# Performance work log

Measured on AMD Instinct MI355X. Metric: run time of the kernel, lower is better.

Reference implementation:

```python
import jax, jax.numpy as jnp
import numpy as np

B, C, H, W = 8, 256, 64, 64
CM = C // 4          # mask channels (theta/phi out) = 64
CI = C - CM          # img channels = 192
EPS = 1e-5


def setup_inputs() -> dict:
    key = jax.random.key(0)
    ks = jax.random.split(key, 12)
    return {
        "x": jax.random.normal(ks[0], (B, C, H, W), dtype=jnp.float32),
        "g_w": jax.random.normal(ks[1], (C, C), dtype=jnp.float32) * 0.05,
        "g_b": jax.random.normal(ks[2], (C,), dtype=jnp.float32) * 0.01,
        "theta_w": jax.random.normal(ks[3], (CM, CM), dtype=jnp.float32) * 0.1,
        "theta_b": jax.random.normal(ks[4], (CM,), dtype=jnp.float32) * 0.01,
        "phi_w": jax.random.normal(ks[5], (CM, CI), dtype=jnp.float32) * 0.06,
        "phi_b": jax.random.normal(ks[6], (CM,), dtype=jnp.float32) * 0.01,
        "W_w": jax.random.normal(ks[7], (C, C), dtype=jnp.float32) * 0.05,
        "W_b": jax.random.normal(ks[8], (C,), dtype=jnp.float32) * 0.01,
        "bn_gamma": jax.random.normal(ks[9], (C,), dtype=jnp.float32) * 0.1 + 1.0,
        "bn_beta": jax.random.normal(ks[10], (C,), dtype=jnp.float32) * 0.01,
        "bn_mean": jax.random.normal(ks[11], (C,), dtype=jnp.float32) * 0.1,
        "bn_var": jnp.ones((C,), dtype=jnp.float32),
    }


def _conv1x1(t, w, b):
    # [B,Cin,H,W] x [Cout,Cin] -> [B,Cout,H,W]
    return jnp.einsum('bchw,oc->bohw', t, w) + b[None, :, None, None]


def _maxpool2(t):
    b, c, h, w = t.shape
    return t.reshape(b, c, h // 2, 2, w // 2, 2).max(axis=(3, 5))


def reference(x, g_w, g_b, theta_w, theta_b, phi_w, phi_b, W_w, W_b,
              bn_gamma, bn_beta, bn_mean, bn_var):
    b, c, h, w = x.shape
    ci = c // 4
    mask_ch = x[:, :ci]          # [B, C/4, H, W]
    img_ch = x[:, ci:]           # [B, 3C/4, H, W]

    # g: conv1x1 then 2x2 maxpool -> [B, C, N'] -> [B, N', C]
    g_x = _maxpool2(_conv1x1(x, g_w, g_b)).reshape(b, c, -1).transpose(0, 2, 1)
    # theta: conv1x1 on mask -> [B, N, C/4]
    theta_x = _conv1x1(mask_ch, theta_w, theta_b).reshape(b, ci, -1).transpose(0, 2, 1)
    # phi: conv1x1 on img then pool -> [B, C/4, N']
    phi_x = _maxpool2(_conv1x1(img_ch, phi_w, phi_b)).reshape(b, ci, -1)

    f = jnp.einsum('bnc,bcm->bnm', theta_x, phi_x)     # [B, N, N']
    f_div_C = jax.nn.softmax(f, axis=-1)
    y = jnp.einsum('bnm,bmc->bnc', f_div_C, g_x)       # [B, N, C]
    y = y.transpose(0, 2, 1).reshape(b, c, h, w)

    W_y = _conv1x1(y, W_w, W_b)
    # BatchNorm (inference form with running stats)
    inv = jax.lax.rsqrt(bn_var + EPS)
    W_y = (W_y - bn_mean[None, :, None, None]) * (inv * bn_gamma)[None, :, None, None] \
          + bn_beta[None, :, None, None]
    return W_y + x
```

## Files before the change

### kernel.cpp

```cpp
#include <hip/hip_runtime.h>
#include <hip/hip_bf16.h>

typedef __hip_bfloat16 bf16;
typedef unsigned short ushort;
typedef unsigned int uint;
typedef __attribute__((ext_vector_type(8))) short short8;
typedef __attribute__((ext_vector_type(4))) float f32x4;

#define Bn 8
#define Cn 256
#define Nn 4096
#define Mn 1024
#define EPSf 1e-5f

__device__ __forceinline__ float b2f(const bf16 v){ return __bfloat162float(v); }
__device__ __forceinline__ ushort f2bu(float f){
  uint u = __float_as_uint(f);
  return (ushort)((u + 0x7FFFu + ((u >> 16) & 1u)) >> 16);
}


__global__ __launch_bounds__(256) void transpose_kernel(
    const float* __restrict__ x, bf16* __restrict__ xT)
{
  __shared__ float xs[64][65];
  const int t = threadIdx.x;
  const int p0 = blockIdx.x*64, c0 = blockIdx.y*64, b = blockIdx.z;
  #pragma unroll
  for (int i = 0; i < 16; ++i) {
    int idx = t + i*256; int cl = idx >> 6, pl = idx & 63;
    xs[cl][pl] = x[((long)(b*Cn) + c0 + cl)*Nn + p0 + pl];
  }
  __syncthreads();
  ushort* xTu = (ushort*)xT;
  #pragma unroll
  for (int i = 0; i < 8; ++i) {
    int idx = t + i*256; int pl = idx >> 5, cp = idx & 31;
    uint u = (uint)f2bu(xs[cp*2][pl]) | ((uint)f2bu(xs[cp*2+1][pl]) << 16);
    *(uint*)(xTu + ((long)(b*Nn) + p0 + pl)*Cn + c0 + cp*2) = u;
  }
}

__global__ __launch_bounds__(256) void wcomb_kernel(
    const float* __restrict__ tw, const float* __restrict__ tb,
    const float* __restrict__ pw, const float* __restrict__ pb,
    const float* __restrict__ gw, const float* __restrict__ gb,
    bf16* __restrict__ Wcomb, float* __restrict__ bcomb)
{
  const int r = blockIdx.x, c = threadIdx.x;
  float v;
  if (r < 64)        v = (c < 64)  ? tw[r*64 + c]            : 0.f;
  else if (r < 128)  v = (c >= 64) ? pw[(r-64)*192 + (c-64)] : 0.f;
  else               v = gw[(r-128)*256 + c];
  Wcomb[r*256 + c] = __float2bfloat16(v);
  if (c == 0)
    bcomb[r] = (r < 64) ? tb[r] : (r < 128) ? pb[r-64] : gb[r-128];
}

__global__ __launch_bounds__(256) void gemm384_kernel(
    const bf16* __restrict__ xT, const bf16* __restrict__ Wcomb,
    const float* __restrict__ bcomb, bf16* __restrict__ Q,
    bf16* __restrict__ K, bf16* __restrict__ Vt)
{
  __shared__ union {
    struct { ushort As[128*40]; ushort Bs[128*40]; } g;
    float Pb[2][128][33];
  } sm;
  const int t = threadIdx.x;
  const int px = blockIdx.x, o0 = blockIdx.y*128, b = blockIdx.z;
  const int p0 = px*128;
  const int lane = t & 63, w = t >> 6;
  const int ql = lane & 15, quad = lane >> 4;
  const int wm = (w & 1)*64, wn = (w >> 1)*64;
  const ushort* xTu = (const ushort*)xT;
  const ushort* Wu  = (const ushort*)Wcomb;

  const int r0 = t >> 2, cq0 = t & 3;
  const int r1 = (t + 256) >> 2, cq1 = (t + 256) & 3;
  const ushort* aSrc0 = xTu + ((long)(b*Nn) + p0 + r0)*Cn + cq0*8;
  const ushort* aSrc1 = xTu + ((long)(b*Nn) + p0 + r1)*Cn + cq1*8;
  const ushort* bSrc0 = Wu + (o0 + r0)*Cn + cq0*8;
  const ushort* bSrc1 = Wu + (o0 + r1)*Cn + cq1*8;

  f32x4 acc[4][4];
  #pragma unroll
  for (int i = 0; i < 4; ++i)
    #pragma unroll
    for (int j = 0; j < 4; ++j) acc[i][j] = (f32x4){0.f,0.f,0.f,0.f};

  uint4 aReg0 = *(const uint4*)(aSrc0);
  uint4 aReg1 = *(const uint4*)(aSrc1);
  uint4 bReg0 = *(const uint4*)(bSrc0);
  uint4 bReg1 = *(const uint4*)(bSrc1);

  for (int kc = 0; kc < 8; ++kc) {
    __syncthreads();
    *(uint4*)(sm.g.As + r0*40 + cq0*8) = aReg0;
    *(uint4*)(sm.g.As + r1*40 + cq1*8) = aReg1;
    *(uint4*)(sm.g.Bs + r0*40 + cq0*8) = bReg0;
    *(uint4*)(sm.g.Bs + r1*40 + cq1*8) = bReg1;
    __syncthreads();
    if (kc < 7) {
      const int k1 = (kc + 1)*32;
      aReg0 = *(const uint4*)(aSrc0 + k1);
      aReg1 = *(const uint4*)(aSrc1 + k1);
      bReg0 = *(const uint4*)(bSrc0 + k1);
      bReg1 = *(const uint4*)(bSrc1 + k1);
    }
    short8 aF[4], bF[4];
    #pragma unroll
    for (int mi = 0; mi < 4; ++mi)
      aF[mi] = *(const short8*)(sm.g.As + (wm + mi*16 + ql)*40 + quad*8);
    #pragma unroll
    for (int ni = 0; ni < 4; ++ni)
      bF[ni] = *(const short8*)(sm.g.Bs + (wn + ni*16 + ql)*40 + quad*8);
    #pragma unroll
    for (int mi = 0; mi < 4; ++mi)
      #pragma unroll
      for (int ni = 0; ni < 4; ++ni)
        acc[mi][ni] = __builtin_amdgcn_mfma_f32_16x16x32_bf16(aF[mi], bF[ni], acc[mi][ni], 0, 0, 0);
  }
  float bias[4];
  #pragma unroll
  for (int ni = 0; ni < 4; ++ni) bias[ni] = bcomb[o0 + wn + ni*16 + ql];

  if (o0 == 0 && wn == 0) {
    #pragma unroll
    for (int mi = 0; mi < 4; ++mi)
      #pragma unroll
      for (int ni = 0; ni < 4; ++ni)
        #pragma unroll
        for (int r = 0; r < 4; ++r) {
          int p = p0 + wm + mi*16 + quad*4 + r;
          Q[((long)(b*Nn) + p)*64 + ni*16 + ql] = __float2bfloat16(acc[mi][ni][r] + bias[ni]);
        }
  }
  __syncthreads();
  if (o0 != 0 || wn == 64) {
    int g = w & 1;
    #pragma unroll
    for (int mi = 0; mi < 4; ++mi)
      #pragma unroll
      for (int ni = 0; ni < 4; ++ni) {
        float a0 = acc[mi][ni][0] + bias[ni], a1 = acc[mi][ni][1] + bias[ni];
        float a2 = acc[mi][ni][2] + bias[ni], a3 = acc[mi][ni][3] + bias[ni];
        int o = wn + ni*16 + ql;
        int wp = mi*8 + quad*2;
        sm.Pb[g][o][wp]     = fmaxf(a0, a1);
        sm.Pb[g][o][wp + 1] = fmaxf(a2, a3);
      }
  }
  __syncthreads();
  if (o0 == 0) {
    int wp = t & 31, og = t >> 5;
    ushort kv[8];
    #pragma unroll
    for (int j = 0; j < 8; ++j) {
      int o = 64 + og*8 + j;
      kv[j] = f2bu(fmaxf(sm.Pb[0][o][wp], sm.Pb[1][o][wp]));
    }
    long kidx = ((long)(b*64) + px*2 + (wp>>4))*1024 + (og>>2)*512
              + ((og&3)*16 + (wp&15))*8;
    *(uint4*)((ushort*)K + kidx) = *(uint4*)kv;
  } else {
    int ol = t >> 1, wp0 = (t & 1)*16;
    ushort vv[16];
    #pragma unroll
    for (int j = 0; j < 16; ++j)
      vv[j] = f2bu(fmaxf(sm.Pb[0][ol][wp0 + j], sm.Pb[1][ol][wp0 + j]));
    int n = (o0 - 128) + ol;
    long vbase = (long)(b)*262144 + (px>>1)*16384 + (n>>4)*1024 + (px&1)*512;
    ushort* dst0 = (ushort*)Vt + vbase + ((wp0>>3)*16 + (n&15))*8;
    *(uint4*)dst0         = *(uint4*)(vv);
    *(uint4*)(dst0 + 128) = *(uint4*)(vv + 8);
  }
}

__global__ __launch_bounds__(512) void attn_kernel(
    const bf16* __restrict__ Q, const bf16* __restrict__ K, const bf16* __restrict__ Vt,
    bf16* __restrict__ Y)
{
  __shared__ __align__(16) ushort Ps[2][64*68];
  __shared__ float l_sh[2][64];

  const int t = threadIdx.x;
  const int b = blockIdx.y, q0 = blockIdx.x*64;
  const int lane = t & 63, w = t >> 6;
  const int ql = lane & 15, quad = lane >> 4;
  const int rt = w & 3;
  const int kh = w >> 2;
  const int rh = (w & 1)*32;
  const int cq = (w >> 1)*64;
  const ushort* Qu = (const ushort*)Q;
  const ushort* Ku = (const ushort*)K;
  const ushort* Vu = (const ushort*)Vt;

  const long qrow = (long)(b*Nn) + q0 + rt*16 + ql;
  short8 aQ0 = *(const short8*)(Qu + qrow*64 + quad*8);
  short8 aQ1 = *(const short8*)(Qu + qrow*64 + 32 + quad*8);

  const ushort* kfp = Ku + ((long)(b*64) + kh*2)*1024 + lane*8;
  const ushort* vfp = Vu + (long)(b)*262144 + (cq>>4)*1024 + lane*8;

  float lrow[4];
  #pragma unroll
  for (int r = 0; r < 4; ++r) lrow[r] = 0.f;

  f32x4 acc[2][4];
  #pragma unroll
  for (int mi = 0; mi < 2; ++mi)
    #pragma unroll
    for (int ci = 0; ci < 4; ++ci) acc[mi][ci] = (f32x4){0.f,0.f,0.f,0.f};

  short8 kf[4], vf[8];
  auto LD_K = [&](int mt){
    #pragma unroll
    for (int ct = 0; ct < 2; ++ct)
      #pragma unroll
      for (int hf = 0; hf < 2; ++hf)
        kf[ct*2+hf] = *(const short8*)(kfp + mt*4096 + ct*1024 + hf*512);
  };
  auto LD_V = [&](int mt){
    #pragma unroll
    for (int ci = 0; ci < 4; ++ci)
      #pragma unroll
      for (int hf = 0; hf < 2; ++hf)
        vf[ci*2+hf] = *(const short8*)(vfp + mt*16384 + ci*1024 + hf*512);
  };
  auto QK = [&](int sel){
    #pragma unroll
    for (int ct = 0; ct < 2; ++ct) {
      int kb = kh*32 + ct*16;
      f32x4 s = (f32x4){0.f,0.f,0.f,0.f};
      s = __builtin_amdgcn_mfma_f32_16x16x32_bf16(aQ0, kf[ct*2],   s, 0, 0, 0);
      s = __builtin_amdgcn_mfma_f32_16x16x32_bf16(aQ1, kf[ct*2+1], s, 0, 0, 0);
      #pragma unroll
      for (int r = 0; r < 4; ++r) {
        float e = __expf(s[r]);
        lrow[r] += e;
        Ps[sel][(rt*16 + quad*4 + r)*68 + kb + ql] = f2bu(e);
      }
    }
  };
  auto PV = [&](int sel){
    short8 aP0[2], aP1[2];
    #pragma unroll
    for (int mi = 0; mi < 2; ++mi) {
      aP0[mi] = *(const short8*)(&Ps[sel][(rh + mi*16 + ql)*68 + quad*8]);
      aP1[mi] = *(const short8*)(&Ps[sel][(rh + mi*16 + ql)*68 + 32 + quad*8]);
    }
    #pragma unroll
    for (int ci = 0; ci < 4; ++ci)
      #pragma unroll
      for (int mi = 0; mi < 2; ++mi) {
        acc[mi][ci] = __builtin_amdgcn_mfma_f32_16x16x32_bf16(aP0[mi], vf[ci*2],   acc[mi][ci], 0, 0, 0);
        acc[mi][ci] = __builtin_amdgcn_mfma_f32_16x16x32_bf16(aP1[mi], vf[ci*2+1], acc[mi][ci], 0, 0, 0);
      }
  };

  LD_K(0);
  LD_V(0);
  QK(0);
  LD_K(1);
  __syncthreads();

  for (int mt = 1; mt < 16; ++mt) {
    PV((mt-1)&1);
    LD_V(mt);
    QK(mt&1);
    LD_K((mt+1)&15);
    __syncthreads();
  }
  PV(1);

  #pragma unroll
  for (int r = 0; r < 4; ++r)
    #pragma unroll
    for (int off = 1; off < 16; off <<= 1)
      lrow[r] += __shfl_xor(lrow[r], off, 64);
  if (ql == 0) {
    #pragma unroll
    for (int r = 0; r < 4; ++r) l_sh[kh][rt*16 + quad*4 + r] = lrow[r];
  }
  __syncthreads();
  #pragma unroll
  for (int mi = 0; mi < 2; ++mi)
    #pragma unroll
    for (int r = 0; r < 4; ++r) {
      int row = rh + mi*16 + quad*4 + r;
      float inv = 1.f / (l_sh[0][row] + l_sh[1][row]);
      #pragma unroll
      for (int ci = 0; ci < 4; ++ci)
        Y[((long)(b*Nn) + q0 + row)*256 + cq + ci*16 + ql] = __float2bfloat16(acc[mi][ci][r]*inv);
    }
}

__global__ __launch_bounds__(256) void wconv_kernel(
    const bf16* __restrict__ Y, const float* __restrict__ Ww, const float* __restrict__ Wb,
    const float* __restrict__ gamma, const float* __restrict__ beta,
    const float* __restrict__ mean, const float* __restrict__ var,
    const float* __restrict__ x, float* __restrict__ out)
{
  __shared__ __align__(16) ushort As[128*40];
  __shared__ __align__(16) ushort Bs[128*40];
  __shared__ float ssc[128], ssh[128];
  const int t = threadIdx.x;
  const int n0 = blockIdx.x*128, o0 = blockIdx.y*128, b = blockIdx.z;
  const int lane = t & 63, w = t >> 6;
  const int ql = lane & 15, quad = lane >> 4;
  const int wm = (w & 1)*64, wn = (w >> 1)*64;
  const ushort* Yu = (const ushort*)Y;

  if (t < 128) {
    int o = o0 + t;
    float sc = gamma[o] * rsqrtf(var[o] + EPSf);
    ssc[t] = sc;
    ssh[t] = (Wb[o] - mean[o])*sc + beta[o];
  }

  const int ar[4] = { t >> 3, (t+256) >> 3, (t+512) >> 3, (t+768) >> 3 };
  const int ac[4] = { t & 7,  (t+256) & 7,  (t+512) & 7,  (t+768) & 7 };
  const int br0 = t >> 2, bc0 = t & 3;
  const int br1 = (t+256) >> 2, bc1 = (t+256) & 3;
  const float* aSrc[4] = {
    Ww + (o0 + ar[0])*Cn + ac[0]*4, Ww + (o0 + ar[1])*Cn + ac[1]*4,
    Ww + (o0 + ar[2])*Cn + ac[2]*4, Ww + (o0 + ar[3])*Cn + ac[3]*4 };
  const ushort* bSrc0 = Yu + ((long)(b*Nn) + n0 + br0)*Cn + bc0*8;
  const ushort* bSrc1 = Yu + ((long)(b*Nn) + n0 + br1)*Cn + bc1*8;

  f32x4 acc[4][4];
  #pragma unroll
  for (int i = 0; i < 4; ++i)
    #pragma unroll
    for (int j = 0; j < 4; ++j) acc[i][j] = (f32x4){0.f,0.f,0.f,0.f};

  float4 aReg[4];
  #pragma unroll
  for (int i = 0; i < 4; ++i) aReg[i] = *(const float4*)(aSrc[i]);
  uint4 bReg0 = *(const uint4*)(bSrc0);
  uint4 bReg1 = *(const uint4*)(bSrc1);

  for (int kc = 0; kc < 8; ++kc) {
    __syncthreads();
    #pragma unroll
    for (int i = 0; i < 4; ++i) {
      uint lo = (uint)f2bu(aReg[i].x) | ((uint)f2bu(aReg[i].y) << 16);
      uint hi = (uint)f2bu(aReg[i].z) | ((uint)f2bu(aReg[i].w) << 16);
      *(uint2*)(As + ar[i]*40 + ac[i]*4) = make_uint2(lo, hi);
    }
    *(uint4*)(Bs + br0*40 + bc0*8) = bReg0;
    *(uint4*)(Bs + br1*40 + bc1*8) = bReg1;
    __syncthreads();
    if (kc < 7) {
      const int k1 = (kc + 1)*32;
      #pragma unroll
      for (int i = 0; i < 4; ++i) aReg[i] = *(const float4*)(aSrc[i] + k1);
      bReg0 = *(const uint4*)(bSrc0 + k1);
      bReg1 = *(const uint4*)(bSrc1 + k1);
    }
    short8 aF[4], bF[4];
    #pragma unroll
    for (int mi = 0; mi < 4; ++mi)
      aF[mi] = *(const short8*)(As + (wm + mi*16 + ql)*40 + quad*8);
    #pragma unroll
    for (int ni = 0; ni < 4; ++ni)
      bF[ni] = *(const short8*)(Bs + (wn + ni*16 + ql)*40 + quad*8);
    #pragma unroll
    for (int mi = 0; mi < 4; ++mi)
      #pragma unroll
      for (int ni = 0; ni < 4; ++ni)
        acc[mi][ni] = __builtin_amdgcn_mfma_f32_16x16x32_bf16(aF[mi], bF[ni], acc[mi][ni], 0, 0, 0);
  }
  #pragma unroll
  for (int mi = 0; mi < 4; ++mi)
    #pragma unroll
    for (int r = 0; r < 4; ++r) {
      int ol = wm + mi*16 + quad*4 + r;
      int o = o0 + ol;
      float sc = ssc[ol], sh = ssh[ol];
      #pragma unroll
      for (int ni = 0; ni < 4; ++ni) {
        int n = n0 + wn + ni*16 + ql;
        long gidx = ((long)(b*Cn + o))*Nn + n;
        out[gidx] = acc[mi][ni][r]*sc + sh + x[gidx];
      }
    }
}

extern "C" void kernel_launch(void* const* d_in, const int* in_sizes, int n_in,
                              void* d_out, int out_size, void* d_ws, size_t ws_size,
                              hipStream_t stream)
{
  const float* x       = (const float*)d_in[0];
  const float* g_w     = (const float*)d_in[1];
  const float* g_b     = (const float*)d_in[2];
  const float* theta_w = (const float*)d_in[3];
  const float* theta_b = (const float*)d_in[4];
  const float* phi_w   = (const float*)d_in[5];
  const float* phi_b   = (const float*)d_in[6];
  const float* W_w     = (const float*)d_in[7];
  const float* W_b     = (const float*)d_in[8];
  const float* bn_g    = (const float*)d_in[9];
  const float* bn_b    = (const float*)d_in[10];
  const float* bn_m    = (const float*)d_in[11];
  const float* bn_v    = (const float*)d_in[12];
  float* out = (float*)d_out;

  bf16* wsb = (bf16*)d_ws;
  bf16* xT    = wsb;
  bf16* Y     = wsb;
  bf16* Q     = wsb + 8388608;
  bf16* K     = wsb + 10485760;
  bf16* Vt    = wsb + 11010048;
  bf16* Wcomb = wsb + 13107200;
  float* bcomb = (float*)(wsb + 13205504);

  transpose_kernel<<<dim3(64, 4, Bn), 256, 0, stream>>>(x, xT);
  wcomb_kernel<<<dim3(384), 256, 0, stream>>>(theta_w, theta_b, phi_w, phi_b, g_w, g_b, Wcomb, bcomb);
  gemm384_kernel<<<dim3(32, 3, Bn), 256, 0, stream>>>(xT, Wcomb, bcomb, Q, K, Vt);
  attn_kernel<<<dim3(64, Bn), 512, 0, stream>>>(Q, K, Vt, Y);
  wconv_kernel<<<dim3(32, 2, Bn), 256, 0, stream>>>(Y, W_w, W_b, bn_g, bn_b, bn_m, bn_v, x, out);
}
```

Measured before the change: 174.7 us.

## Store GEMM operands in MFMA fragment-tiled layout and load fragments directly from global

```diff
diff --git a/kernel.cpp b/kernel.cpp
--- a/kernel.cpp
+++ b/kernel.cpp
@@ -32,12 +32,20 @@
     xs[cl][pl] = x[((long)(b*Cn) + c0 + cl)*Nn + p0 + pl];
   }
   __syncthreads();
-  ushort* xTu = (ushort*)xT;
-  #pragma unroll
-  for (int i = 0; i < 8; ++i) {
-    int idx = t + i*256; int pl = idx >> 5, cp = idx & 31;
-    uint u = (uint)f2bu(xs[cp*2][pl]) | ((uint)f2bu(xs[cp*2+1][pl]) << 16);
-    *(uint*)(xTu + ((long)(b*Nn) + p0 + pl)*Cn + c0 + cp*2) = u;
+  ushort* xt = (ushort*)xT;
+  const int ql = t & 15, quad = (t >> 4) & 3, w = t >> 6;
+  #pragma unroll
+  for (int i = 0; i < 2; ++i) {
+    int f = w + i*4;
+    int p16f = f >> 1, kcf = f & 1;
+    int pl = p16f*16 + ql;
+    int ch0 = kcf*32 + quad*8;
+    uint u[4];
+    #pragma unroll
+    for (int k = 0; k < 4; ++k)
+      u[k] = (uint)f2bu(xs[ch0 + 2*k][pl]) | ((uint)f2bu(xs[ch0 + 2*k + 1][pl]) << 16);
+    long base = ((long)b*2048 + ((p0>>4) + p16f)*8 + (c0>>5) + kcf)*512;
+    *(uint4*)(xt + base + (t & 63)*8) = make_uint4(u[0], u[1], u[2], u[3]);
   }
 }
 
@@ -52,35 +60,42 @@
   if (r < 64)        v = (c < 64)  ? tw[r*64 + c]            : 0.f;
   else if (r < 128)  v = (c >= 64) ? pw[(r-64)*192 + (c-64)] : 0.f;
   else               v = gw[(r-128)*256 + c];
-  Wcomb[r*256 + c] = __float2bfloat16(v);
+  ((ushort*)Wcomb)[((r>>4)*8 + (c>>5))*512 + (((c&31)>>3)*16 + (r&15))*8 + (c&7)]
+      = f2bu(v);
   if (c == 0)
     bcomb[r] = (r < 64) ? tb[r] : (r < 128) ? pb[r-64] : gb[r-128];
 }
 
+__global__ __launch_bounds__(256) void wwt_kernel(
+    const float* __restrict__ Ww, bf16* __restrict__ Wwt)
+{
+  const int r = blockIdx.x, c = threadIdx.x;
+  ((ushort*)Wwt)[((r>>4)*8 + (c>>5))*512 + (((c&31)>>3)*16 + (r&15))*8 + (c&7)]
+      = f2bu(Ww[r*256 + c]);
+}
+
 __global__ __launch_bounds__(256) void gemm384_kernel(
-    const bf16* __restrict__ xT, const bf16* __restrict__ Wcomb,
+    const bf16* __restrict__ xTt, const bf16* __restrict__ Wct,
     const float* __restrict__ bcomb, bf16* __restrict__ Q,
     bf16* __restrict__ K, bf16* __restrict__ Vt)
 {
-  __shared__ union {
-    struct { ushort As[128*40]; ushort Bs[128*40]; } g;
-    float Pb[2][128][33];
-  } sm;
+  __shared__ float Pb[2][128][33];
   const int t = threadIdx.x;
   const int px = blockIdx.x, o0 = blockIdx.y*128, b = blockIdx.z;
   const int p0 = px*128;
   const int lane = t & 63, w = t >> 6;
   const int ql = lane & 15, quad = lane >> 4;
   const int wm = (w & 1)*64, wn = (w >> 1)*64;
-  const ushort* xTu = (const ushort*)xT;
-  const ushort* Wu  = (const ushort*)Wcomb;
-
-  const int r0 = t >> 2, cq0 = t & 3;
-  const int r1 = (t + 256) >> 2, cq1 = (t + 256) & 3;
-  const ushort* aSrc0 = xTu + ((long)(b*Nn) + p0 + r0)*Cn + cq0*8;
-  const ushort* aSrc1 = xTu + ((long)(b*Nn) + p0 + r1)*Cn + cq1*8;
-  const ushort* bSrc0 = Wu + (o0 + r0)*Cn + cq0*8;
-  const ushort* bSrc1 = Wu + (o0 + r1)*Cn + cq1*8;
+  const ushort* xu = (const ushort*)xTt;
+  const ushort* wu = (const ushort*)Wct;
+
+  const ushort* aB[4]; const ushort* bB[4];
+  #pragma unroll
+  for (int mi = 0; mi < 4; ++mi)
+    aB[mi] = xu + (((long)b*256 + px*8 + (wm>>4) + mi)*8)*512 + lane*8;
+  #pragma unroll
+  for (int ni = 0; ni < 4; ++ni)
+    bB[ni] = wu + ((long)(((o0 + wn)>>4) + ni)*8)*512 + lane*8;
 
   f32x4 acc[4][4];
   #pragma unroll
@@ -88,38 +103,42 @@
     #pragma unroll
     for (int j = 0; j < 4; ++j) acc[i][j] = (f32x4){0.f,0.f,0.f,0.f};
 
-  uint4 aReg0 = *(const uint4*)(aSrc0);
-  uint4 aReg1 = *(const uint4*)(aSrc1);
-  uint4 bReg0 = *(const uint4*)(bSrc0);
-  uint4 bReg1 = *(const uint4*)(bSrc1);
-
-  for (int kc = 0; kc < 8; ++kc) {
-    __syncthreads();
-    *(uint4*)(sm.g.As + r0*40 + cq0*8) = aReg0;
-    *(uint4*)(sm.g.As + r1*40 + cq1*8) = aReg1;
-    *(uint4*)(sm.g.Bs + r0*40 + cq0*8) = bReg0;
-    *(uint4*)(sm.g.Bs + r1*40 + cq1*8) = bReg1;
-    __syncthreads();
-    if (kc < 7) {
-      const int k1 = (kc + 1)*32;
-      aReg0 = *(const uint4*)(aSrc0 + k1);
-      aReg1 = *(const uint4*)(aSrc1 + k1);
-      bReg0 = *(const uint4*)(bSrc0 + k1);
-      bReg1 = *(const uint4*)(bSrc1 + k1);
-    }
-    short8 aF[4], bF[4];
-    #pragma unroll
-    for (int mi = 0; mi < 4; ++mi)
-      aF[mi] = *(const short8*)(sm.g.As + (wm + mi*16 + ql)*40 + quad*8);
-    #pragma unroll
-    for (int ni = 0; ni < 4; ++ni)
-      bF[ni] = *(const short8*)(sm.g.Bs + (wn + ni*16 + ql)*40 + quad*8);
+  short8 aX[4], bX[4], aY[4], bY[4];
+  #pragma unroll
+  for (int i = 0; i < 4; ++i) {
+    aX[i] = *(const short8*)(aB[i]);
+    bX[i] = *(const short8*)(bB[i]);
+    aY[i] = *(const short8*)(aB[i] + 512);
+    bY[i] = *(const short8*)(bB[i] + 512);
+  }
+  #pragma unroll
+  for (int kc2 = 0; kc2 < 4; ++kc2) {
     #pragma unroll
     for (int mi = 0; mi < 4; ++mi)
       #pragma unroll
       for (int ni = 0; ni < 4; ++ni)
-        acc[mi][ni] = __builtin_amdgcn_mfma_f32_16x16x32_bf16(aF[mi], bF[ni], acc[mi][ni], 0, 0, 0);
-  }
+        acc[mi][ni] = __builtin_amdgcn_mfma_f32_16x16x32_bf16(aX[mi], bX[ni], acc[mi][ni], 0, 0, 0);
+    if (kc2 < 3) {
+      #pragma unroll
+      for (int i = 0; i < 4; ++i) {
+        aX[i] = *(const short8*)(aB[i] + (kc2*2 + 2)*512);
+        bX[i] = *(const short8*)(bB[i] + (kc2*2 + 2)*512);
+      }
+    }
+    #pragma unroll
+    for (int mi = 0; mi < 4; ++mi)
+      #pragma unroll
+      for (int ni = 0; ni < 4; ++ni)
+        acc[mi][ni] = __builtin_amdgcn_mfma_f32_16x16x32_bf16(aY[mi], bY[ni], acc[mi][ni], 0, 0, 0);
+    if (kc2 < 3) {
+      #pragma unroll
+      for (int i = 0; i < 4; ++i) {
+        aY[i] = *(const short8*)(aB[i] + (kc2*2 + 3)*512);
+        bY[i] = *(const short8*)(bB[i] + (kc2*2 + 3)*512);
+      }
+    }
+  }
+
   float bias[4];
   #pragma unroll
   for (int ni = 0; ni < 4; ++ni) bias[ni] = bcomb[o0 + wn + ni*16 + ql];
@@ -146,8 +165,8 @@
         float a2 = acc[mi][ni][2] + bias[ni], a3 = acc[mi][ni][3] + bias[ni];
         int o = wn + ni*16 + ql;
         int wp = mi*8 + quad*2;
-        sm.Pb[g][o][wp]     = fmaxf(a0, a1);
-        sm.Pb[g][o][wp + 1] = fmaxf(a2, a3);
+        Pb[g][o][wp]     = fmaxf(a0, a1);
+        Pb[g][o][wp + 1] = fmaxf(a2, a3);
       }
   }
   __syncthreads();
@@ -157,7 +176,7 @@
     #pragma unroll
     for (int j = 0; j < 8; ++j) {
       int o = 64 + og*8 + j;
-      kv[j] = f2bu(fmaxf(sm.Pb[0][o][wp], sm.Pb[1][o][wp]));
+      kv[j] = f2bu(fmaxf(Pb[0][o][wp], Pb[1][o][wp]));
     }
     long kidx = ((long)(b*64) + px*2 + (wp>>4))*1024 + (og>>2)*512
               + ((og&3)*16 + (wp&15))*8;
@@ -167,7 +186,7 @@
     ushort vv[16];
     #pragma unroll
     for (int j = 0; j < 16; ++j)
-      vv[j] = f2bu(fmaxf(sm.Pb[0][ol][wp0 + j], sm.Pb[1][ol][wp0 + j]));
+      vv[j] = f2bu(fmaxf(Pb[0][ol][wp0 + j], Pb[1][ol][wp0 + j]));
     int n = (o0 - 128) + ol;
     long vbase = (long)(b)*262144 + (px>>1)*16384 + (n>>4)*1024 + (px&1)*512;
     ushort* dst0 = (ushort*)Vt + vbase + ((wp0>>3)*16 + (n&15))*8;
@@ -283,33 +302,36 @@
     for (int r = 0; r < 4; ++r) l_sh[kh][rt*16 + quad*4 + r] = lrow[r];
   }
   __syncthreads();
+  ushort* Yu = (ushort*)Y;
   #pragma unroll
   for (int mi = 0; mi < 2; ++mi)
     #pragma unroll
     for (int r = 0; r < 4; ++r) {
       int row = rh + mi*16 + quad*4 + r;
       float inv = 1.f / (l_sh[0][row] + l_sh[1][row]);
-      #pragma unroll
-      for (int ci = 0; ci < 4; ++ci)
-        Y[((long)(b*Nn) + q0 + row)*256 + cq + ci*16 + ql] = __float2bfloat16(acc[mi][ci][r]*inv);
+      int n = q0 + row;
+      #pragma unroll
+      for (int ci = 0; ci < 4; ++ci) {
+        int c = cq + ci*16 + ql;
+        long idx = (((long)b*256 + (n>>4))*8 + (c>>5))*512
+                 + (((c&31)>>3)*16 + (n&15))*8 + (c&7);
+        Yu[idx] = f2bu(acc[mi][ci][r]*inv);
+      }
     }
 }
 
 __global__ __launch_bounds__(256) void wconv_kernel(
-    const bf16* __restrict__ Y, const float* __restrict__ Ww, const float* __restrict__ Wb,
+    const bf16* __restrict__ Yt, const bf16* __restrict__ Wwt, const float* __restrict__ Wb,
     const float* __restrict__ gamma, const float* __restrict__ beta,
     const float* __restrict__ mean, const float* __restrict__ var,
     const float* __restrict__ x, float* __restrict__ out)
 {
-  __shared__ __align__(16) ushort As[128*40];
-  __shared__ __align__(16) ushort Bs[128*40];
   __shared__ float ssc[128], ssh[128];
   const int t = threadIdx.x;
   const int n0 = blockIdx.x*128, o0 = blockIdx.y*128, b = blockIdx.z;
   const int lane = t & 63, w = t >> 6;
   const int ql = lane & 15, quad = lane >> 4;
   const int wm = (w & 1)*64, wn = (w >> 1)*64;
-  const ushort* Yu = (const ushort*)Y;
 
   if (t < 128) {
     int o = o0 + t;
@@ -318,15 +340,13 @@
     ssh[t] = (Wb[o] - mean[o])*sc + beta[o];
   }
 
-  const int ar[4] = { t >> 3, (t+256) >> 3, (t+512) >> 3, (t+768) >> 3 };
-  const int ac[4] = { t & 7,  (t+256) & 7,  (t+512) & 7,  (t+768) & 7 };
-  const int br0 = t >> 2, bc0 = t & 3;
-  const int br1 = (t+256) >> 2, bc1 = (t+256) & 3;
-  const float* aSrc[4] = {
-    Ww + (o0 + ar[0])*Cn + ac[0]*4, Ww + (o0 + ar[1])*Cn + ac[1]*4,
-    Ww + (o0 + ar[2])*Cn + ac[2]*4, Ww + (o0 + ar[3])*Cn + ac[3]*4 };
-  const ushort* bSrc0 = Yu + ((long)(b*Nn) + n0 + br0)*Cn + bc0*8;
-  const ushort* bSrc1 = Yu + ((long)(b*Nn) + n0 + br1)*Cn + bc1*8;
+  const ushort* aB[4]; const ushort* bB[4];
+  #pragma unroll
+  for (int mi = 0; mi < 4; ++mi)
+    aB[mi] = (const ushort*)Wwt + ((long)(((o0 + wm)>>4) + mi)*8)*512 + lane*8;
+  #pragma unroll
+  for (int ni = 0; ni < 4; ++ni)
+    bB[ni] = (const ushort*)Yt + (((long)b*256 + ((n0 + wn)>>4) + ni)*8)*512 + lane*8;
 
   f32x4 acc[4][4];
   #pragma unroll
@@ -334,43 +354,42 @@
     #pragma unroll
     for (int j = 0; j < 4; ++j) acc[i][j] = (f32x4){0.f,0.f,0.f,0.f};
 
-  float4 aReg[4];
-  #pragma unroll
-  for (int i = 0; i < 4; ++i) aReg[i] = *(const float4*)(aSrc[i]);
-  uint4 bReg0 = *(const uint4*)(bSrc0);
-  uint4 bReg1 = *(const uint4*)(bSrc1);
-
-  for (int kc = 0; kc < 8; ++kc) {
-    __syncthreads();
-    #pragma unroll
-    for (int i = 0; i < 4; ++i) {
-      uint lo = (uint)f2bu(aReg[i].x) | ((uint)f2bu(aReg[i].y) << 16);
-      uint hi = (uint)f2bu(aReg[i].z) | ((uint)f2bu(aReg[i].w) << 16);
-      *(uint2*)(As + ar[i]*40 + ac[i]*4) = make_uint2(lo, hi);
-    }
-    *(uint4*)(Bs + br0*40 + bc0*8) = bReg0;
-    *(uint4*)(Bs + br1*40 + bc1*8) = bReg1;
-    __syncthreads();
-    if (kc < 7) {
-      const int k1 = (kc + 1)*32;
-      #pragma unroll
-      for (int i = 0; i < 4; ++i) aReg[i] = *(const float4*)(aSrc[i] + k1);
-      bReg0 = *(const uint4*)(bSrc0 + k1);
-      bReg1 = *(const uint4*)(bSrc1 + k1);
-    }
-    short8 aF[4], bF[4];
-    #pragma unroll
-    for (int mi = 0; mi < 4; ++mi)
-      aF[mi] = *(const short8*)(As + (wm + mi*16 + ql)*40 + quad*8);
-    #pragma unroll
-    for (int ni = 0; ni < 4; ++ni)
-      bF[ni] = *(const short8*)(Bs + (wn + ni*16 + ql)*40 + quad*8);
+  short8 aX[4], bX[4], aY[4], bY[4];
+  #pragma unroll
+  for (int i = 0; i < 4; ++i) {
+    aX[i] = *(const short8*)(aB[i]);
+    bX[i] = *(const short8*)(bB[i]);
+    aY[i] = *(const short8*)(aB[i] + 512);
+    bY[i] = *(const short8*)(bB[i] + 512);
+  }
+  #pragma unroll
+  for (int kc2 = 0; kc2 < 4; ++kc2) {
     #pragma unroll
     for (int mi = 0; mi < 4; ++mi)
       #pragma unroll
       for (int ni = 0; ni < 4; ++ni)
-        acc[mi][ni] = __builtin_amdgcn_mfma_f32_16x16x32_bf16(aF[mi], bF[ni], acc[mi][ni], 0, 0, 0);
-  }
+        acc[mi][ni] = __builtin_amdgcn_mfma_f32_16x16x32_bf16(aX[mi], bX[ni], acc[mi][ni], 0, 0, 0);
+    if (kc2 < 3) {
+      #pragma unroll
+      for (int i = 0; i < 4; ++i) {
+        aX[i] = *(const short8*)(aB[i] + (kc2*2 + 2)*512);
+        bX[i] = *(const short8*)(bB[i] + (kc2*2 + 2)*512);
+      }
+    }
+    #pragma unroll
+    for (int mi = 0; mi < 4; ++mi)
+      #pragma unroll
+      for (int ni = 0; ni < 4; ++ni)
+        acc[mi][ni] = __builtin_amdgcn_mfma_f32_16x16x32_bf16(aY[mi], bY[ni], acc[mi][ni], 0, 0, 0);
+    if (kc2 < 3) {
+      #pragma unroll
+      for (int i = 0; i < 4; ++i) {
+        aY[i] = *(const short8*)(aB[i] + (kc2*2 + 3)*512);
+        bY[i] = *(const short8*)(bB[i] + (kc2*2 + 3)*512);
+      }
+    }
+  }
+  __syncthreads();
   #pragma unroll
   for (int mi = 0; mi < 4; ++mi)
     #pragma unroll
@@ -407,17 +426,19 @@
   float* out = (float*)d_out;
 
   bf16* wsb = (bf16*)d_ws;
-  bf16* xT    = wsb;
-  bf16* Y     = wsb;
+  bf16* xTt   = wsb;
+  bf16* Yt    = wsb;
   bf16* Q     = wsb + 8388608;
   bf16* K     = wsb + 10485760;
   bf16* Vt    = wsb + 11010048;
-  bf16* Wcomb = wsb + 13107200;
+  bf16* Wct   = wsb + 13107200;
   float* bcomb = (float*)(wsb + 13205504);
-
-  transpose_kernel<<<dim3(64, 4, Bn), 256, 0, stream>>>(x, xT);
-  wcomb_kernel<<<dim3(384), 256, 0, stream>>>(theta_w, theta_b, phi_w, phi_b, g_w, g_b, Wcomb, bcomb);
-  gemm384_kernel<<<dim3(32, 3, Bn), 256, 0, stream>>>(xT, Wcomb, bcomb, Q, K, Vt);
-  attn_kernel<<<dim3(64, Bn), 512, 0, stream>>>(Q, K, Vt, Y);
-  wconv_kernel<<<dim3(32, 2, Bn), 256, 0, stream>>>(Y, W_w, W_b, bn_g, bn_b, bn_m, bn_v, x, out);
-}
+  bf16* Wwt   = wsb + 13206272;
+
+  transpose_kernel<<<dim3(64, 4, Bn), 256, 0, stream>>>(x, xTt);
+  wcomb_kernel<<<dim3(384), 256, 0, stream>>>(theta_w, theta_b, phi_w, phi_b, g_w, g_b, Wct, bcomb);
+  wwt_kernel<<<dim3(256), 256, 0, stream>>>(W_w, Wwt);
+  gemm384_kernel<<<dim3(32, 3, Bn), 256, 0, stream>>>(xTt, Wct, bcomb, Q, K, Vt);
+  attn_kernel<<<dim3(64, Bn), 512, 0, stream>>>(Q, K, Vt, Yt);
+  wconv_kernel<<<dim3(32, 2, Bn), 256, 0, stream>>>(Yt, Wwt, W_b, bn_g, bn_b, bn_m, bn_v, x, out);
+}
```

Result: no change. 172.0 us (-1.5%).
